# Optimization experiments

Measured on AMD Instinct MI355X. Metric: run time of the kernel, lower is better.

## Reference

```python
import jax, jax.numpy as jnp
import numpy as np

B, D, M, K = 4096, 768, 100000, 10


def setup_inputs() -> dict:
    key = jax.random.key(0)
    k1, k2 = jax.random.split(key)
    x = jax.random.normal(k1, (B, D), dtype=jnp.float32)
    evidence_embeddings = jax.random.normal(k2, (M, D), dtype=jnp.float32)
    return {"x": x, "evidence_embeddings": evidence_embeddings, "k": K}


def reference(x, evidence_embeddings, k):
    # cos_sim = x @ E^T  -> [B, M]
    cos_sim = jnp.einsum("bd,md->bm", x, evidence_embeddings)
    # top-k along evidence dim (dim=1)
    scores, indices = jax.lax.top_k(cos_sim, k)
    return scores, indices
```

## Files before the change

### kernel.cpp

```cpp
#include <hip/hip_runtime.h>
#include <hip/hip_fp8.h>
#include <math.h>
#include <stdint.h>

#define B_ROWS 4096
#define D_DIM  768
#define M_ROWS 100000
#define K_TOP  10

#define KSTEPS 48
#define E32N   3125
#define B32N   128
#define NGRP   16
#define NBB    16
#define NITER_TOT 391
#define CAND   12
#define KCN    12
#define LTK    5
#define TILEB  24576

typedef long i64;
typedef float f32x16 __attribute__((ext_vector_type(16)));

#define XF_BYTES (128ull * TILEB)
#define EF_OFF   XF_BYTES
#define EF_BYTES (3125ull * TILEB)
#define CS_OFF   (EF_OFF + EF_BYTES)
#define CS_BYTES (4096ull * NGRP * CAND * 4)
#define CI_OFF   (CS_OFF + CS_BYTES)
#define CI_BYTES (4096ull * NGRP * CAND * 4)
#define WS_NEED  (CI_OFF + CI_BYTES)

__global__ __launch_bounds__(256) void convert_frag8(
    const float* __restrict__ src, uint8_t* __restrict__ dst, int nband)
{
  int tid  = blockIdx.x * 256 + threadIdx.x;
  int l    = tid & 63;
  int rest = tid >> 6;
  int ks   = rest % KSTEPS;
  int band = rest / KSTEPS;
  if (band >= nband) return;
  int row = band * 32 + (l & 31);
  int k0  = ks * 16 + 8 * (l >> 5);
  const float* s = src + (size_t)row * D_DIM + k0;
  float4 v0 = *(const float4*)s;
  float4 v1 = *(const float4*)(s + 4);
  float f0 = v0.x, f1 = v0.y, f2 = v0.z, f3 = v0.w;
  float f4 = v1.x, f5 = v1.y, f6 = v1.z, f7 = v1.w;
  unsigned long long o = 0;
  o |= (unsigned long long)(__hip_fp8_e4m3(f0).__x) << 0;
  o |= (unsigned long long)(__hip_fp8_e4m3(f1).__x) << 8;
  o |= (unsigned long long)(__hip_fp8_e4m3(f2).__x) << 16;
  o |= (unsigned long long)(__hip_fp8_e4m3(f3).__x) << 24;
  o |= (unsigned long long)(__hip_fp8_e4m3(f4).__x) << 32;
  o |= (unsigned long long)(__hip_fp8_e4m3(f5).__x) << 40;
  o |= (unsigned long long)(__hip_fp8_e4m3(f6).__x) << 48;
  o |= (unsigned long long)(__hip_fp8_e4m3(f7).__x) << 56;
  *(unsigned long long*)(dst + ((size_t)(band * KSTEPS + ks) << 9) + l * 8) = o;
}

__device__ __forceinline__ void ins5(float (&ts)[LTK], int (&ti)[LTK],
                                     float s, int idx)
{
  ts[LTK - 1] = s; ti[LTK - 1] = idx;
#pragma unroll
  for (int q = LTK - 1; q > 0; --q) {
    if (ts[q] > ts[q - 1]) {
      float a = ts[q]; ts[q] = ts[q - 1]; ts[q - 1] = a;
      int   b = ti[q]; ti[q] = ti[q - 1]; ti[q - 1] = b;
    }
  }
}

__device__ __forceinline__ float max16(const f32x16& v)
{
  float a = fmaxf(fmaxf(v[0], v[1]), fmaxf(v[2], v[3]));
  float b = fmaxf(fmaxf(v[4], v[5]), fmaxf(v[6], v[7]));
  float c = fmaxf(fmaxf(v[8], v[9]), fmaxf(v[10], v[11]));
  float d = fmaxf(fmaxf(v[12], v[13]), fmaxf(v[14], v[15]));
  return fmaxf(fmaxf(a, b), fmaxf(c, d));
}

__device__ __forceinline__ void gll16(const void* src, void* dst)
{
  __builtin_amdgcn_global_load_lds(
      (const __attribute__((address_space(1))) void*)(uintptr_t)src,
      (__attribute__((address_space(3))) void*)(uint32_t)(uintptr_t)dst,
      16, 0, 0);
}

__global__ __launch_bounds__(1024, 4) void gemm_topk(
    const uint8_t* __restrict__ Ef, const uint8_t* __restrict__ Xf,
    float* __restrict__ cs, int* __restrict__ ci)
{
  __shared__ char lds[2][40960];

  const int t    = threadIdx.x;
  const int lane = t & 63;
  const int w    = t >> 6;
  const int ew   = w >> 2;
  const int bw   = w & 3;

  const int id = blockIdx.x;
  const int g  = (id & 7) + 8 * (id >> 7);
  const int bb = (id >> 3) & 15;
  const int niter = 24 + (g < (NITER_TOT - 16 * 24) ? 1 : 0);

  const bool isE = (w < 8);
  char* dst0 = &lds[0][0] + w * 2048 + lane * 16;
  char* dst1 = &lds[1][0] + w * 2048 + lane * 16;

  const uint8_t* xsrc = Xf + (size_t)(bb * 8 + (w - 8)) * TILEB + lane * 16;

  const char* rb0p = &lds[0][0] + lane * 8;
  const char* rb1p = &lds[1][0] + lane * 8;

  float ts0[LTK], ts1[LTK]; int ti0[LTK], ti1[LTK];
#pragma unroll
  for (int q = 0; q < LTK; ++q) {
    ts0[q] = -INFINITY; ts1[q] = -INFINITY;
    ti0[q] = 0x7fffffff; ti1[q] = 0x7fffffff;
  }

#pragma unroll 1
  for (int j = 0; j < niter; ++j) {
    const int e32base = (g + NGRP * j) * 8;

    const uint8_t* sp;
    if (isE) {
      int e32 = e32base + w; if (e32 > E32N - 1) e32 = E32N - 1;
      sp = Ef + (size_t)e32 * TILEB + lane * 16;
    } else {
      sp = xsrc;
    }

    f32x16 acc0[2], acc1[2];
#pragma unroll
    for (int e = 0; e < 2; ++e) {
#pragma unroll
      for (int q = 0; q < 16; ++q) { acc0[e][q] = 0.f; acc1[e][q] = 0.f; }
    }

    gll16(sp, dst0);
    gll16(sp + 1024, dst0 + 1024);
    const uint8_t* sc = sp + 2048;

#pragma unroll 1
    for (int kc = 0; kc < KCN; ++kc) {
      asm volatile("s_waitcnt vmcnt(0)" ::: "memory");
      __builtin_amdgcn_s_barrier();

      const char* rp = (kc & 1) ? rb1p : rb0p;
      char* dp = (kc & 1) ? dst0 : dst1;

      if (kc < KCN - 1) {
        gll16(sc, dp);
        gll16(sc + 1024, dp + 1024);
        sc += 2048;
      }

#pragma unroll
      for (int kk = 0; kk < 4; ++kk) {
        i64 a[2], b[2];
#pragma unroll
        for (int e = 0; e < 2; ++e)
          a[e] = *(const i64*)(rp + ((ew * 2 + e) * 2048 + kk * 512));
#pragma unroll
        for (int x2 = 0; x2 < 2; ++x2)
          b[x2] = *(const i64*)(rp + ((8 + bw * 2 + x2) * 2048 + kk * 512));
#pragma unroll
        for (int e = 0; e < 2; ++e) {
          acc0[e] = __builtin_amdgcn_mfma_f32_32x32x16_fp8_fp8(a[e], b[0], acc0[e], 0, 0, 0);
          acc1[e] = __builtin_amdgcn_mfma_f32_32x32x16_fp8_fp8(a[e], b[1], acc1[e], 0, 0, 0);
        }
      }
    }

#pragma unroll
    for (int e = 0; e < 2; ++e) {
      const int ebase = e32base * 32 + (ew * 2 + e) * 32 + 4 * (lane >> 5);
      if (max16(acc0[e]) > ts0[LTK - 1]) {
#pragma unroll
        for (int q = 0; q < 16; ++q) {
          int eidx = ebase + (q & 3) + 8 * (q >> 2);
          float s = acc0[e][q];
          if (eidx < M_ROWS && s > ts0[LTK - 1]) ins5(ts0, ti0, s, eidx);
        }
      }
      if (max16(acc1[e]) > ts1[LTK - 1]) {
#pragma unroll
        for (int q = 0; q < 16; ++q) {
          int eidx = ebase + (q & 3) + 8 * (q >> 2);
          float s = acc1[e][q];
          if (eidx < M_ROWS && s > ts1[LTK - 1]) ins5(ts1, ti1, s, eidx);
        }
      }
    }
  }

  __syncthreads();
  float* ds = (float*)&lds[0][0];
  int*   di = (int*)&lds[1][0];
  {
    int half = lane >> 5, cl = lane & 31;
    int base0 = ((((ew * 2 + half) * 4 + bw) * 2 + 0) * 32 + cl) * LTK;
    int base1 = ((((ew * 2 + half) * 4 + bw) * 2 + 1) * 32 + cl) * LTK;
#pragma unroll
    for (int q = 0; q < LTK; ++q) {
      ds[base0 + q] = ts0[q]; di[base0 + q] = ti0[q];
      ds[base1 + q] = ts1[q]; di[base1 + q] = ti1[q];
    }
  }
  __syncthreads();
  if (t < 256) {
    int c = t; int bw2 = c >> 6, bt2 = (c >> 5) & 1, cl2 = c & 31;
    int hb[8];
#pragma unroll
    for (int u = 0; u < 8; ++u) {
      int ew2 = u >> 1, h2 = u & 1;
      hb[u] = ((((ew2 * 2 + h2) * 4 + bw2) * 2 + bt2) * 32 + cl2) * LTK;
    }
    const int row = bb * 256 + c;
    float* ocs = cs + ((size_t)row * NGRP + g) * CAND;
    int*   oci = ci + ((size_t)row * NGRP + g) * CAND;
    for (int o = 0; o < CAND; ++o) {
      float best = -INFINITY; int bidx = 0x7fffffff; int bu = 0, bq = 0;
#pragma unroll
      for (int u = 0; u < 8; ++u) {
        for (int q = 0; q < LTK; ++q) {
          float s = ds[hb[u] + q]; int id2 = di[hb[u] + q];
          if (s > best || (s == best && id2 < bidx)) { best = s; bidx = id2; bu = u; bq = q; }
        }
      }
      ds[hb[bu] + bq] = -INFINITY;
      ocs[o] = best; oci[o] = bidx;
    }
  }
}

__global__ __launch_bounds__(64) void final_merge(
    const float* __restrict__ x, const float* __restrict__ E,
    const float* __restrict__ cs, const int* __restrict__ ci,
    float* __restrict__ out)
{
  __shared__ float ls[192]; __shared__ int li[192];
  __shared__ int c32[32]; __shared__ double rs[32];
  const int row = blockIdx.x;
  const int lane = threadIdx.x;
  for (int q = lane; q < 192; q += 64) {
    ls[q] = cs[(size_t)row * 192 + q];
    li[q] = ci[(size_t)row * 192 + q];
  }
  __syncthreads();

  for (int o = 0; o < 32; ++o) {
    float bs = -INFINITY; int bi = 0x7fffffff; int bp = 0;
    for (int q = lane; q < 192; q += 64) {
      float s = ls[q];
      if (s > bs || (s == bs && li[q] < bi)) { bs = s; bi = li[q]; bp = q; }
    }
#pragma unroll
    for (int mk = 1; mk <= 32; mk <<= 1) {
      float qs = __shfl_xor(bs, mk, 64);
      int   qi = __shfl_xor(bi, mk, 64);
      int   qp = __shfl_xor(bp, mk, 64);
      if (qs > bs || (qs == bs && qi < bi)) { bs = qs; bi = qi; bp = qp; }
    }
    if (lane == 0) { c32[o] = bi; ls[bp] = -INFINITY; }
    __syncthreads();
  }

  {
    int cd = lane >> 1, p = lane & 1;
    int cid = c32[cd];
    if ((unsigned)cid >= M_ROWS) cid = 0;
    const float* Er = E + (size_t)cid * D_DIM + p * 384;
    const float* Xr = x + (size_t)row * D_DIM + p * 384;
    double s = 0.0;
#pragma unroll 8
    for (int d = 0; d < 384; ++d) s += (double)Xr[d] * (double)Er[d];
    s += __shfl_xor(s, 1, 64);
    if (p == 0) rs[cd] = s;
  }
  __syncthreads();

  if (lane == 0) {
    for (int o = 0; o < K_TOP; ++o) {
      double bs = rs[0]; int bc = c32[0]; int b = 0;
      for (int q = 1; q < 32; ++q) {
        double v = rs[q]; int cq = c32[q];
        if (v > bs || (v == bs && cq < bc)) { bs = v; bc = cq; b = q; }
      }
      out[(size_t)row * K_TOP + o] = (float)bs;
      out[(size_t)B_ROWS * K_TOP + (size_t)row * K_TOP + o] = (float)bc;
      rs[b] = -1.0e300;
    }
  }
}

#define RB   16
#define GQ   64
#define MMF  4
#define NJ   391
#define NTF  1024
#define XPAD 772
#define DQ4  192

__global__ __launch_bounds__(NTF, 4) void retr_fused(
    const float* __restrict__ x, const float* __restrict__ E,
    float* __restrict__ out)
{
  __shared__ float smem[21248];
  const int t = threadIdx.x;
  const int r = t & 15;
  const int g = t >> 4;
  const int rb0 = blockIdx.x * RB;
  {
    const float4* xg = (const float4*)(x + (size_t)rb0 * D_DIM);
    for (int q = t; q < RB * DQ4; q += NTF) {
      int row = q / DQ4, c4 = q % DQ4;
      float4 v = xg[q];
      *(float4*)(smem + row * XPAD + c4 * 4) = v;
    }
  }
  __syncthreads();
  float ts[K_TOP]; int ti[K_TOP];
#pragma unroll
  for (int q = 0; q < K_TOP; ++q) { ts[q] = -INFINITY; ti[q] = 0x7fffffff; }
  const float4* xr4 = (const float4*)(smem + r * XPAD);
  for (int j = 0; j < NJ; ++j) {
    const int m0 = (g + (j << 6)) * MMF;
    const float4* ep[MMF];
#pragma unroll
    for (int mm = 0; mm < MMF; ++mm) {
      int ml = m0 + mm;
      int mc = (ml < M_ROWS) ? ml : (M_ROWS - 1);
      ep[mm] = (const float4*)(E + (size_t)mc * D_DIM);
    }
    float4 acc[MMF];
#pragma unroll
    for (int mm = 0; mm < MMF; ++mm) acc[mm] = make_float4(0.f, 0.f, 0.f, 0.f);
#pragma unroll 4
    for (int dq = 0; dq < DQ4; ++dq) {
      float4 xv = xr4[dq];
#pragma unroll
      for (int mm = 0; mm < MMF; ++mm) {
        float4 e = ep[mm][dq];
        acc[mm].x += e.x * xv.x; acc[mm].y += e.y * xv.y;
        acc[mm].z += e.z * xv.z; acc[mm].w += e.w * xv.w;
      }
    }
#pragma unroll
    for (int mm = 0; mm < MMF; ++mm) {
      int ml = m0 + mm;
      float s = (acc[mm].x + acc[mm].y) + (acc[mm].z + acc[mm].w);
      if (ml < M_ROWS && s > ts[K_TOP - 1]) {
        ts[K_TOP - 1] = s; ti[K_TOP - 1] = ml;
#pragma unroll
        for (int q = K_TOP - 1; q > 0; --q) {
          if (ts[q] > ts[q - 1]) {
            float tf = ts[q]; ts[q] = ts[q - 1]; ts[q - 1] = tf;
            int   tq = ti[q]; ti[q] = ti[q - 1]; ti[q - 1] = tq;
          }
        }
      }
    }
  }
  __syncthreads();
  float*  cs  = smem;
  int*    ci  = (int*)(smem + 10240);
  int*    cnd = (int*)(smem + 20480);
  double* rsd = (double*)(smem + 20736);
#pragma unroll
  for (int q = 0; q < K_TOP; ++q) {
    cs[(r * GQ + g) * K_TOP + q] = ts[q];
    ci[(r * GQ + g) * K_TOP + q] = ti[q];
  }
  __syncthreads();
  const int w = t >> 6;
  const int lane = t & 63;
  {
    float ms[K_TOP]; int mi[K_TOP];
#pragma unroll
    for (int q = 0; q < K_TOP; ++q) {
      ms[q] = cs[(w * GQ + lane) * K_TOP + q];
      mi[q] = ci[(w * GQ + lane) * K_TOP + q];
    }
    for (int o = 0; o < 16; ++o) {
      float hs = ms[0]; int hi = mi[0];
      float bs = hs;    int bi = hi;
#pragma unroll
      for (int mk = 1; mk <= 32; mk <<= 1) {
        float qs = __shfl_xor(bs, mk, 64);
        int   qi = __shfl_xor(bi, mk, 64);
        if (qs > bs || (qs == bs && qi < bi)) { bs = qs; bi = qi; }
      }
      bool win = (hs == bs) && (hi == bi);
      if (win) {
#pragma unroll
        for (int q = 0; q < K_TOP - 1; ++q) { ms[q] = ms[q + 1]; mi[q] = mi[q + 1]; }
        ms[K_TOP - 1] = -INFINITY; mi[K_TOP - 1] = 0x7fffffff;
      }
      if (lane == 0) cnd[w * 16 + o] = bi;
    }
  }
  __syncthreads();
  {
    int cand = lane >> 2, p = lane & 3;
    int cid = cnd[w * 16 + cand];
    const float* Er = E + (size_t)cid * D_DIM + p * 192;
    const float* Xr = x + (size_t)(rb0 + w) * D_DIM + p * 192;
    double s = 0.0;
#pragma unroll 8
    for (int d = 0; d < 192; ++d) s += (double)Xr[d] * (double)Er[d];
    s += __shfl_xor(s, 1, 64);
    s += __shfl_xor(s, 2, 64);
    if (p == 0) rsd[w * 16 + cand] = s;
  }
  __syncthreads();
  if (lane == 0) {
    const int row = rb0 + w;
    for (int o = 0; o < K_TOP; ++o) {
      double bsv = rsd[w * 16 + 0]; int bci = cnd[w * 16 + 0]; int b = 0;
      for (int q = 1; q < 16; ++q) {
        double v = rsd[w * 16 + q]; int c = cnd[w * 16 + q];
        if (v > bsv || (v == bsv && c < bci)) { bsv = v; bci = c; b = q; }
      }
      out[(size_t)row * K_TOP + o] = (float)bsv;
      out[(size_t)B_ROWS * K_TOP + (size_t)row * K_TOP + o] = (float)bci;
      rsd[w * 16 + b] = -1.0e300;
    }
  }
}

extern "C" void kernel_launch(void* const* d_in, const int* in_sizes, int n_in,
                              void* d_out, int out_size, void* d_ws, size_t ws_size,
                              hipStream_t stream) {
  const float* x = (const float*)d_in[0];
  const float* E = (const float*)d_in[1];
  float* out = (float*)d_out;

  if (ws_size < WS_NEED) {
    retr_fused<<<dim3(B_ROWS / RB), NTF, 0, stream>>>(x, E, out);
    return;
  }

  uint8_t* Xfp = (uint8_t*)d_ws;
  uint8_t* Efp = (uint8_t*)((char*)d_ws + EF_OFF);
  float*   csp = (float*)((char*)d_ws + CS_OFF);
  int*     cip = (int*)((char*)d_ws + CI_OFF);

  convert_frag8<<<dim3((B32N * KSTEPS * 64) / 256), 256, 0, stream>>>(x, Xfp, B32N);
  convert_frag8<<<dim3((E32N * KSTEPS * 64) / 256), 256, 0, stream>>>(E, Efp, E32N);
  gemm_topk<<<dim3(NBB * NGRP), 1024, 0, stream>>>(Efp, Xfp, csp, cip);
  final_merge<<<dim3(B_ROWS), 64, 0, stream>>>(x, E, csp, cip, out);
}
```

Before: 828.8 us.

## Triple-buffer LDS tiles with continuous prefetch across output iterations

Replaces the double-buffered LDS staging with three rotating buffers and a global chunk counter, so loads are issued two chunks ahead and prefetching continues across iteration boundaries. The wait becomes vmcnt(2) instead of draining all loads each step, letting one chunk's global-to-LDS copy overlap compute. This removes the pipeline bubble at the start of each j-iteration. Each block now uses 96 KB of LDS instead of 80 KB.

```diff
diff --git a/kernel.cpp b/kernel.cpp
--- a/kernel.cpp
+++ b/kernel.cpp
@@ -93,7 +93,7 @@
     const uint8_t* __restrict__ Ef, const uint8_t* __restrict__ Xf,
     float* __restrict__ cs, int* __restrict__ ci)
 {
-  __shared__ char lds[2][40960];
+  __shared__ char lds[3][32768];
 
   const int t    = threadIdx.x;
   const int lane = t & 63;
@@ -105,15 +105,26 @@
   const int g  = (id & 7) + 8 * (id >> 7);
   const int bb = (id >> 3) & 15;
   const int niter = 24 + (g < (NITER_TOT - 16 * 24) ? 1 : 0);
+  const int CTOT  = niter * KCN;
 
   const bool isE = (w < 8);
-  char* dst0 = &lds[0][0] + w * 2048 + lane * 16;
-  char* dst1 = &lds[1][0] + w * 2048 + lane * 16;
+  const uint32_t doff = (uint32_t)w * 2048 + lane * 16;
 
   const uint8_t* xsrc = Xf + (size_t)(bb * 8 + (w - 8)) * TILEB + lane * 16;
 
-  const char* rb0p = &lds[0][0] + lane * 8;
-  const char* rb1p = &lds[1][0] + lane * 8;
+  auto STAGE = [&](int c, char* bufp) {
+    const int j2  = c / KCN;
+    const int kc2 = c - j2 * KCN;
+    const uint8_t* sp;
+    if (isE) {
+      int e32 = (g + NGRP * j2) * 8 + w; if (e32 > E32N - 1) e32 = E32N - 1;
+      sp = Ef + (size_t)e32 * TILEB + kc2 * 2048 + lane * 16;
+    } else {
+      sp = xsrc + kc2 * 2048;
+    }
+    gll16(sp,        bufp + doff);
+    gll16(sp + 1024, bufp + doff + 1024);
+  };
 
   float ts0[LTK], ts1[LTK]; int ti0[LTK], ti1[LTK];
 #pragma unroll
@@ -122,18 +133,18 @@
     ti0[q] = 0x7fffffff; ti1[q] = 0x7fffffff;
   }
 
+  char* cur = &lds[0][0];
+  char* nxt = &lds[1][0];
+  char* spr = &lds[2][0];
+
+  STAGE(0, cur);
+  STAGE(1, nxt);
+
+  int c = 0;
 #pragma unroll 1
   for (int j = 0; j < niter; ++j) {
     const int e32base = (g + NGRP * j) * 8;
 
-    const uint8_t* sp;
-    if (isE) {
-      int e32 = e32base + w; if (e32 > E32N - 1) e32 = E32N - 1;
-      sp = Ef + (size_t)e32 * TILEB + lane * 16;
-    } else {
-      sp = xsrc;
-    }
-
     f32x16 acc0[2], acc1[2];
 #pragma unroll
     for (int e = 0; e < 2; ++e) {
@@ -141,24 +152,15 @@
       for (int q = 0; q < 16; ++q) { acc0[e][q] = 0.f; acc1[e][q] = 0.f; }
     }
 
-    gll16(sp, dst0);
-    gll16(sp + 1024, dst0 + 1024);
-    const uint8_t* sc = sp + 2048;
-
 #pragma unroll 1
-    for (int kc = 0; kc < KCN; ++kc) {
-      asm volatile("s_waitcnt vmcnt(0)" ::: "memory");
+    for (int kc = 0; kc < KCN; ++kc, ++c) {
+      if (c + 1 < CTOT) { asm volatile("s_waitcnt vmcnt(2)" ::: "memory"); }
+      else              { asm volatile("s_waitcnt vmcnt(0)" ::: "memory"); }
       __builtin_amdgcn_s_barrier();
 
-      const char* rp = (kc & 1) ? rb1p : rb0p;
-      char* dp = (kc & 1) ? dst0 : dst1;
-
-      if (kc < KCN - 1) {
-        gll16(sc, dp);
-        gll16(sc + 1024, dp + 1024);
-        sc += 2048;
-      }
-
+      if (c + 2 < CTOT) STAGE(c + 2, spr);
+
+      const char* rp = cur + lane * 8;
 #pragma unroll
       for (int kk = 0; kk < 4; ++kk) {
         i64 a[2], b[2];
@@ -174,6 +176,8 @@
           acc1[e] = __builtin_amdgcn_mfma_f32_32x32x16_fp8_fp8(a[e], b[1], acc1[e], 0, 0, 0);
         }
       }
+
+      char* tmp = cur; cur = nxt; nxt = spr; spr = tmp;
     }
 
 #pragma unroll
@@ -200,7 +204,7 @@
 
   __syncthreads();
   float* ds = (float*)&lds[0][0];
-  int*   di = (int*)&lds[1][0];
+  int*   di = (int*)(&lds[0][0] + 49152);
   {
     int half = lane >> 5, cl = lane & 31;
     int base0 = ((((ew * 2 + half) * 4 + bw) * 2 + 0) * 32 + cl) * LTK;
@@ -213,14 +217,14 @@
   }
   __syncthreads();
   if (t < 256) {
-    int c = t; int bw2 = c >> 6, bt2 = (c >> 5) & 1, cl2 = c & 31;
+    int cth = t; int bw2 = cth >> 6, bt2 = (cth >> 5) & 1, cl2 = cth & 31;
     int hb[8];
 #pragma unroll
     for (int u = 0; u < 8; ++u) {
       int ew2 = u >> 1, h2 = u & 1;
       hb[u] = ((((ew2 * 2 + h2) * 4 + bw2) * 2 + bt2) * 32 + cl2) * LTK;
     }
-    const int row = bb * 256 + c;
+    const int row = bb * 256 + cth;
     float* ocs = cs + ((size_t)row * NGRP + g) * CAND;
     int*   oci = ci + ((size_t)row * NGRP + g) * CAND;
     for (int o = 0; o < CAND; ++o) {
```

Measured after the change: 945.2 us. +14.0%, slower.

## Split gemm_topk into smaller 512-thread blocks with more evidence groups

Applied to the files above, without the earlier changes.

The fused fp8 GEMM+top-k kernel moves from 1024-thread blocks (8 E waves, 8 E tiles per iteration) to 512-thread blocks (4 E waves, 4 X waves each loading two X tiles). Evidence groups grow from 16 to 48, so 768 blocks are launched instead of 256, and each block keeps 6 candidates per row instead of 12. The aim is better occupancy and load balance across CUs and XCDs. In exchange, the X tile is reloaded more often per evidence tile, and the final merge has more candidates per row to scan (288 instead of 192).

```diff
diff --git a/kernel.cpp b/kernel.cpp
--- a/kernel.cpp
+++ b/kernel.cpp
@@ -11,10 +11,10 @@
 #define KSTEPS 48
 #define E32N   3125
 #define B32N   128
-#define NGRP   16
+#define NGRP   48
 #define NBB    16
-#define NITER_TOT 391
-#define CAND   12
+#define NIT4   782
+#define CAND   6
 #define KCN    12
 #define LTK    5
 #define TILEB  24576
@@ -45,17 +45,15 @@
   const float* s = src + (size_t)row * D_DIM + k0;
   float4 v0 = *(const float4*)s;
   float4 v1 = *(const float4*)(s + 4);
-  float f0 = v0.x, f1 = v0.y, f2 = v0.z, f3 = v0.w;
-  float f4 = v1.x, f5 = v1.y, f6 = v1.z, f7 = v1.w;
   unsigned long long o = 0;
-  o |= (unsigned long long)(__hip_fp8_e4m3(f0).__x) << 0;
-  o |= (unsigned long long)(__hip_fp8_e4m3(f1).__x) << 8;
-  o |= (unsigned long long)(__hip_fp8_e4m3(f2).__x) << 16;
-  o |= (unsigned long long)(__hip_fp8_e4m3(f3).__x) << 24;
-  o |= (unsigned long long)(__hip_fp8_e4m3(f4).__x) << 32;
-  o |= (unsigned long long)(__hip_fp8_e4m3(f5).__x) << 40;
-  o |= (unsigned long long)(__hip_fp8_e4m3(f6).__x) << 48;
-  o |= (unsigned long long)(__hip_fp8_e4m3(f7).__x) << 56;
+  o |= (unsigned long long)(__hip_fp8_e4m3(v0.x).__x) << 0;
+  o |= (unsigned long long)(__hip_fp8_e4m3(v0.y).__x) << 8;
+  o |= (unsigned long long)(__hip_fp8_e4m3(v0.z).__x) << 16;
+  o |= (unsigned long long)(__hip_fp8_e4m3(v0.w).__x) << 24;
+  o |= (unsigned long long)(__hip_fp8_e4m3(v1.x).__x) << 32;
+  o |= (unsigned long long)(__hip_fp8_e4m3(v1.y).__x) << 40;
+  o |= (unsigned long long)(__hip_fp8_e4m3(v1.z).__x) << 48;
+  o |= (unsigned long long)(__hip_fp8_e4m3(v1.w).__x) << 56;
   *(unsigned long long*)(dst + ((size_t)(band * KSTEPS + ks) << 9) + l * 8) = o;
 }
 
@@ -89,11 +87,11 @@
       16, 0, 0);
 }
 
-__global__ __launch_bounds__(1024, 4) void gemm_topk(
+__global__ __launch_bounds__(512, 6) void gemm_topk(
     const uint8_t* __restrict__ Ef, const uint8_t* __restrict__ Xf,
     float* __restrict__ cs, int* __restrict__ ci)
 {
-  __shared__ char lds[2][40960];
+  __shared__ char lds[2][24576];
 
   const int t    = threadIdx.x;
   const int lane = t & 63;
@@ -101,19 +99,32 @@
   const int ew   = w >> 2;
   const int bw   = w & 3;
 
-  const int id = blockIdx.x;
-  const int g  = (id & 7) + 8 * (id >> 7);
-  const int bb = (id >> 3) & 15;
-  const int niter = 24 + (g < (NITER_TOT - 16 * 24) ? 1 : 0);
-
-  const bool isE = (w < 8);
-  char* dst0 = &lds[0][0] + w * 2048 + lane * 16;
-  char* dst1 = &lds[1][0] + w * 2048 + lane * 16;
-
-  const uint8_t* xsrc = Xf + (size_t)(bb * 8 + (w - 8)) * TILEB + lane * 16;
-
-  const char* rb0p = &lds[0][0] + lane * 8;
-  const char* rb1p = &lds[1][0] + lane * 8;
+  const int id  = blockIdx.x;
+  const int xcd = id & 7;
+  const int q8  = id >> 3;
+  const int bb  = q8 & 15;
+  const int g   = xcd * 6 + (q8 >> 4);
+  const int niter = 16 + (g < (NIT4 - NGRP * 16) ? 1 : 0);
+
+  const bool isE = (w < 4);
+  const uint32_t dE  = (uint32_t)w * 2048 + lane * 16;
+  const uint32_t dX0 = 8192u + (uint32_t)(2 * (w - 4)) * 2048 + lane * 16;
+  const uint32_t dX1 = dX0 + 2048;
+
+  const uint8_t* xb0 = Xf + (size_t)(bb * 8 + 2 * (w - 4)) * TILEB + lane * 16;
+  const uint8_t* xb1 = xb0 + TILEB;
+
+  auto STAGE = [&](const uint8_t* s0, const uint8_t* s1, char* base) {
+    if (isE) {
+      gll16(s0,        base + dE);
+      gll16(s0 + 1024, base + dE + 1024);
+    } else {
+      gll16(s0,        base + dX0);
+      gll16(s0 + 1024, base + dX0 + 1024);
+      gll16(s1,        base + dX1);
+      gll16(s1 + 1024, base + dX1 + 1024);
+    }
+  };
 
   float ts0[LTK], ts1[LTK]; int ti0[LTK], ti1[LTK];
 #pragma unroll
@@ -122,16 +133,19 @@
     ti0[q] = 0x7fffffff; ti1[q] = 0x7fffffff;
   }
 
+  char* buf0 = &lds[0][0];
+  char* buf1 = &lds[1][0];
+  const char* rb0p = buf0 + lane * 8;
+  const char* rb1p = buf1 + lane * 8;
+
 #pragma unroll 1
   for (int j = 0; j < niter; ++j) {
-    const int e32base = (g + NGRP * j) * 8;
-
-    const uint8_t* sp;
+    const int it = g + NGRP * j;
+
+    const uint8_t* sE = xb0;
     if (isE) {
-      int e32 = e32base + w; if (e32 > E32N - 1) e32 = E32N - 1;
-      sp = Ef + (size_t)e32 * TILEB + lane * 16;
-    } else {
-      sp = xsrc;
+      int e32 = it * 4 + w; if (e32 > E32N - 1) e32 = E32N - 1;
+      sE = Ef + (size_t)e32 * TILEB + lane * 16;
     }
 
     f32x16 acc0[2], acc1[2];
@@ -141,9 +155,10 @@
       for (int q = 0; q < 16; ++q) { acc0[e][q] = 0.f; acc1[e][q] = 0.f; }
     }
 
-    gll16(sp, dst0);
-    gll16(sp + 1024, dst0 + 1024);
-    const uint8_t* sc = sp + 2048;
+    const uint8_t* sc0 = isE ? sE : xb0;
+    const uint8_t* sc1 = xb1;
+    STAGE(sc0, sc1, buf0);
+    sc0 += 2048; sc1 += 2048;
 
 #pragma unroll 1
     for (int kc = 0; kc < KCN; ++kc) {
@@ -151,12 +166,11 @@
       __builtin_amdgcn_s_barrier();
 
       const char* rp = (kc & 1) ? rb1p : rb0p;
-      char* dp = (kc & 1) ? dst0 : dst1;
+      char* dp = (kc & 1) ? buf0 : buf1;
 
       if (kc < KCN - 1) {
-        gll16(sc, dp);
-        gll16(sc + 1024, dp + 1024);
-        sc += 2048;
+        STAGE(sc0, sc1, dp);
+        sc0 += 2048; sc1 += 2048;
       }
 
 #pragma unroll
@@ -167,7 +181,7 @@
           a[e] = *(const i64*)(rp + ((ew * 2 + e) * 2048 + kk * 512));
 #pragma unroll
         for (int x2 = 0; x2 < 2; ++x2)
-          b[x2] = *(const i64*)(rp + ((8 + bw * 2 + x2) * 2048 + kk * 512));
+          b[x2] = *(const i64*)(rp + (8192 + (bw * 2 + x2) * 2048 + kk * 512));
 #pragma unroll
         for (int e = 0; e < 2; ++e) {
           acc0[e] = __builtin_amdgcn_mfma_f32_32x32x16_fp8_fp8(a[e], b[0], acc0[e], 0, 0, 0);
@@ -178,7 +192,7 @@
 
 #pragma unroll
     for (int e = 0; e < 2; ++e) {
-      const int ebase = e32base * 32 + (ew * 2 + e) * 32 + 4 * (lane >> 5);
+      const int ebase = (it * 4 + ew * 2 + e) * 32 + 4 * (lane >> 5);
       if (max16(acc0[e]) > ts0[LTK - 1]) {
 #pragma unroll
         for (int q = 0; q < 16; ++q) {
@@ -200,7 +214,7 @@
 
   __syncthreads();
   float* ds = (float*)&lds[0][0];
-  int*   di = (int*)&lds[1][0];
+  int*   di = (int*)(&lds[0][0] + 24576);
   {
     int half = lane >> 5, cl = lane & 31;
     int base0 = ((((ew * 2 + half) * 4 + bw) * 2 + 0) * 32 + cl) * LTK;
@@ -214,9 +228,9 @@
   __syncthreads();
   if (t < 256) {
     int c = t; int bw2 = c >> 6, bt2 = (c >> 5) & 1, cl2 = c & 31;
-    int hb[8];
-#pragma unroll
-    for (int u = 0; u < 8; ++u) {
+    int hb[4];
+#pragma unroll
+    for (int u = 0; u < 4; ++u) {
       int ew2 = u >> 1, h2 = u & 1;
       hb[u] = ((((ew2 * 2 + h2) * 4 + bw2) * 2 + bt2) * 32 + cl2) * LTK;
     }
@@ -226,7 +240,7 @@
     for (int o = 0; o < CAND; ++o) {
       float best = -INFINITY; int bidx = 0x7fffffff; int bu = 0, bq = 0;
 #pragma unroll
-      for (int u = 0; u < 8; ++u) {
+      for (int u = 0; u < 4; ++u) {
         for (int q = 0; q < LTK; ++q) {
           float s = ds[hb[u] + q]; int id2 = di[hb[u] + q];
           if (s > best || (s == best && id2 < bidx)) { best = s; bidx = id2; bu = u; bq = q; }
@@ -238,24 +252,26 @@
   }
 }
 
+#define NCAND (NGRP * CAND)
+
 __global__ __launch_bounds__(64) void final_merge(
     const float* __restrict__ x, const float* __restrict__ E,
     const float* __restrict__ cs, const int* __restrict__ ci,
     float* __restrict__ out)
 {
-  __shared__ float ls[192]; __shared__ int li[192];
+  __shared__ float ls[NCAND]; __shared__ int li[NCAND];
   __shared__ int c32[32]; __shared__ double rs[32];
   const int row = blockIdx.x;
   const int lane = threadIdx.x;
-  for (int q = lane; q < 192; q += 64) {
-    ls[q] = cs[(size_t)row * 192 + q];
-    li[q] = ci[(size_t)row * 192 + q];
+  for (int q = lane; q < NCAND; q += 64) {
+    ls[q] = cs[(size_t)row * NCAND + q];
+    li[q] = ci[(size_t)row * NCAND + q];
   }
   __syncthreads();
 
   for (int o = 0; o < 32; ++o) {
     float bs = -INFINITY; int bi = 0x7fffffff; int bp = 0;
-    for (int q = lane; q < 192; q += 64) {
+    for (int q = lane; q < NCAND; q += 64) {
       float s = ls[q];
       if (s > bs || (s == bs && li[q] < bi)) { bs = s; bi = li[q]; bp = q; }
     }
@@ -452,6 +468,6 @@
 
   convert_frag8<<<dim3((B32N * KSTEPS * 64) / 256), 256, 0, stream>>>(x, Xfp, B32N);
   convert_frag8<<<dim3((E32N * KSTEPS * 64) / 256), 256, 0, stream>>>(E, Efp, E32N);
-  gemm_topk<<<dim3(NBB * NGRP), 1024, 0, stream>>>(Efp, Xfp, csp, cip);
+  gemm_topk<<<dim3(NBB * NGRP), 512, 0, stream>>>(Efp, Xfp, csp, cip);
   final_merge<<<dim3(B_ROWS), 64, 0, stream>>>(x, E, csp, cip, out);
 }
```

New measurement: 1.662 ms. 2x slower.
